# Optimization experiments

Measured on AMD Instinct MI355X. Metric: run time of the kernel, lower is better.

The kernel has to match this reference:

```python
import jax, jax.numpy as jnp
import numpy as np

NQ, NT, NA = 10000, 50000, 50000
E_GR, E_LT, E_SIM, E_COMP, E_GEN = 50000, 50000, 80000, 100000, 50000
HID, NH, HC, DOT, NL = 512, 4, 128, 256, 2
NEG_SLOPE = 0.2  # PyG GATv2Conv default negative_slope


def _gatv2(x_src, x_dst, src, dst, Wl, bl, Wr, br, att, bias, n_dst):
    # GATv2: x_j = lin_l(x_src), x_i = lin_r(x_dst); e = att . leaky_relu(x_i + x_j)
    xl = (x_src @ Wl + bl).reshape(-1, NH, HC)   # [Ns,H,C]
    xr = (x_dst @ Wr + br).reshape(-1, NH, HC)   # [Nd,H,C]
    m = jax.nn.leaky_relu(xl[src] + xr[dst], NEG_SLOPE)      # [E,H,C]
    logits = jnp.einsum('ehc,hc->eh', m, att)                # [E,H]
    lmax = jax.lax.stop_gradient(jax.ops.segment_max(logits, dst, num_segments=n_dst))
    lmax = jnp.where(jnp.isfinite(lmax), lmax, 0.0)
    ex = jnp.exp(logits - lmax[dst])
    denom = jax.ops.segment_sum(ex, dst, num_segments=n_dst)
    alpha = ex / (denom[dst] + 1e-16)                        # softmax over incoming edges
    out = jax.ops.segment_sum(xl[src] * alpha[:, :, None], dst, num_segments=n_dst)
    return out.reshape(n_dst, NH * HC) + bias


def _layernorm(x, g, b):
    mu = x.mean(-1, keepdims=True)
    var = ((x - mu) ** 2).mean(-1, keepdims=True)
    return (x - mu) / jnp.sqrt(var + 1e-5) * g + b


def _forward(xq, xt, xa, answer_features,
             qp_W, qp_b, tp_W, tp_b, ap_W, ap_b,
             afp_W1, afp_b1, afp_W2, afp_b2,
             conv_Wl, conv_bl, conv_Wr, conv_br, conv_att, conv_bias,
             qh_W, qh_b, qh_g, qh_beta, rh_W, rh_b, rh_g, rh_beta, score_bias,
             ei_gr, ei_lt, ei_sim, ei_comp, ei_gen):
    hq = xq @ qp_W + qp_b
    ht = xt @ tp_W + tp_b
    ha = xa @ ap_W + ap_b
    # add_self_loops=True only for ('query','similar_to','query')
    loops = jnp.arange(NQ, dtype=ei_sim.dtype)
    sim_src = jnp.concatenate([ei_sim[0], loops])
    sim_dst = jnp.concatenate([ei_sim[1], loops])
    for l in range(NL):
        P = lambda r: (conv_Wl[l, r], conv_bl[l, r], conv_Wr[l, r], conv_br[l, r], conv_att[l, r], conv_bias[l, r])
        o_gr = _gatv2(hq, ht, ei_gr[0], ei_gr[1], *P(0), NT)          # query -> think
        o_rgr = _gatv2(ht, hq, ei_gr[1], ei_gr[0], *P(1), NQ)         # think -> query (rev)
        o_lt = _gatv2(ht, ha, ei_lt[0], ei_lt[1], *P(2), NA)          # think -> answer
        o_rlt = _gatv2(ha, ht, ei_lt[1], ei_lt[0], *P(3), NT)         # answer -> think (rev)
        o_sim = _gatv2(hq, hq, sim_src, sim_dst, *P(4), NQ)           # query -> query
        o_cmp = _gatv2(ht, ht, ei_comp[0], ei_comp[1], *P(5), NT)     # think -> think
        # HeteroConv aggr='mean' across relations per destination type, then relu
        hq = jax.nn.relu((o_rgr + o_sim) / 2.0)
        ht = jax.nn.relu((o_gr + o_rlt + o_cmp) / 3.0)
        ha = jax.nn.relu(o_lt)
    q_emb = hq[ei_gen[0]]
    a_emb = ha[ei_gen[1]]
    t_emb = ht[ei_gen[1]]  # faithful to source: think indexed with answer-side index
    af_emb = jax.nn.relu(answer_features @ afp_W1 + afp_b1) @ afp_W2 + afp_b2
    q = _layernorm(q_emb @ qh_W + qh_b, qh_g, qh_beta)
    r = _layernorm(jnp.concatenate([t_emb, a_emb, af_emb], -1) @ rh_W + rh_b, rh_g, rh_beta)
    return (q * r).sum(-1) / jnp.sqrt(jnp.float32(DOT)) + score_bias


def setup_inputs() -> dict:
    ks = jax.random.split(jax.random.key(0), 40)
    n = lambda j, shape, s=0.05: jax.random.normal(ks[j], shape, jnp.float32) * s
    ri = lambda j, shape, hi: jax.random.randint(ks[j], shape, 0, hi, jnp.int32)
    return dict(
        xq=n(0, (NQ, 384), 1.0), xt=n(1, (NT, 384), 1.0), xa=n(2, (NA, 384), 1.0),
        answer_features=n(3, (E_GEN, 6), 1.0),
        qp_W=n(4, (384, HID)), qp_b=n(5, (HID,)),
        tp_W=n(6, (384, HID)), tp_b=n(7, (HID,)),
        ap_W=n(8, (384, HID)), ap_b=n(9, (HID,)),
        afp_W1=n(10, (6, 64)), afp_b1=n(11, (64,)),
        afp_W2=n(12, (64, HID)), afp_b2=n(13, (HID,)),
        conv_Wl=n(14, (NL, 6, HID, HID)), conv_bl=n(15, (NL, 6, HID)),
        conv_Wr=n(16, (NL, 6, HID, HID)), conv_br=n(17, (NL, 6, HID)),
        conv_att=n(18, (NL, 6, NH, HC)), conv_bias=n(19, (NL, 6, HID)),
        qh_W=n(20, (HID, DOT)), qh_b=n(21, (DOT,)),
        qh_g=jnp.ones((DOT,), jnp.float32), qh_beta=jnp.zeros((DOT,), jnp.float32),
        rh_W=n(22, (HID * 3, DOT)), rh_b=n(23, (DOT,)),
        rh_g=jnp.ones((DOT,), jnp.float32), rh_beta=jnp.zeros((DOT,), jnp.float32),
        score_bias=jnp.zeros((1,), jnp.float32),
        ei_gr=jnp.stack([ri(24, (E_GR,), NQ), ri(25, (E_GR,), NT)]),
        ei_lt=jnp.stack([ri(26, (E_LT,), NT), ri(27, (E_LT,), NA)]),
        ei_sim=ri(28, (2, E_SIM), NQ),
        ei_comp=ri(29, (2, E_COMP), NT),
        ei_gen=jnp.stack([ri(30, (E_GEN,), NQ), ri(31, (E_GEN,), NA)]),
    )


def reference(xq, xt, xa, answer_features,
              qp_W, qp_b, tp_W, tp_b, ap_W, ap_b,
              afp_W1, afp_b1, afp_W2, afp_b2,
              conv_Wl, conv_bl, conv_Wr, conv_br, conv_att, conv_bias,
              qh_W, qh_b, qh_g, qh_beta, rh_W, rh_b, rh_g, rh_beta, score_bias,
              ei_gr, ei_lt, ei_sim, ei_comp, ei_gen):
    return _forward(xq, xt, xa, answer_features,
                    qp_W, qp_b, tp_W, tp_b, ap_W, ap_b,
                    afp_W1, afp_b1, afp_W2, afp_b2,
                    conv_Wl, conv_bl, conv_Wr, conv_br, conv_att, conv_bias,
                    qh_W, qh_b, qh_g, qh_beta, rh_W, rh_b, rh_g, rh_beta, score_bias,
                    ei_gr, ei_lt, ei_sim, ei_comp, ei_gen)
```

## Files before the change

kernel.cpp:

```cpp
#include <hip/hip_runtime.h>
#include <cstdio>
#include <type_traits>

#define NQ 10000
#define NT 50000
#define NA 50000
#define E_GR 50000
#define E_LT 50000
#define E_SIM 80000
#define E_COMP 100000
#define E_GEN 50000
#define NEG_SLOPE 0.2f

#define NDTOT 220000
#define NSTOT 220000
#define ETOT  390000
__device__ __constant__ const int c_degOff[7]  = {0, 50000, 60000, 110000, 120000, 170000, 220000};
__device__ __constant__ const int c_sOff[7]    = {0, 10000, 60000, 110000, 120000, 170000, 220000};
__device__ __constant__ const int c_eOff[7]    = {0, 50000, 100000, 150000, 240000, 340000, 390000};
__device__ __constant__ const int c_nb[6]      = {49, 10, 49, 10, 49, 49};
__device__ __constant__ const int c_nbOff[7]   = {0, 49, 59, 108, 118, 167, 216};
__device__ __constant__ const int c_snb[6]     = {10, 49, 49, 10, 49, 49};
__device__ __constant__ const int c_snbOff[7]  = {0, 10, 59, 108, 118, 167, 216};

typedef unsigned short bf16_t;
typedef unsigned int u32;
typedef __attribute__((ext_vector_type(8))) short short8v;
typedef __attribute__((ext_vector_type(4))) float f32x4;

__device__ __forceinline__ float bf2f(u32 bits) { return __uint_as_float(bits << 16); }
__device__ __forceinline__ u32 f2bf(float f) {
  u32 u = __float_as_uint(f);
  return (u + 0x7FFFu + ((u >> 16) & 1u)) >> 16;
}
__device__ __forceinline__ u32 pack2(float a, float b) { return f2bf(a) | (f2bf(b) << 16); }
__device__ __forceinline__ void unpack8(uint4 u, float* f) {
  f[0] = bf2f(u.x & 0xffffu); f[1] = bf2f(u.x >> 16);
  f[2] = bf2f(u.y & 0xffffu); f[3] = bf2f(u.y >> 16);
  f[4] = bf2f(u.z & 0xffffu); f[5] = bf2f(u.z >> 16);
  f[6] = bf2f(u.w & 0xffffu); f[7] = bf2f(u.w >> 16);
}

__device__ __forceinline__ void gload16(const void* g, void* l) {
  __builtin_amdgcn_global_load_lds(
      (const __attribute__((address_space(1))) void*)g,
      (__attribute__((address_space(3))) void*)l, 16, 0, 0);
}

struct GemmDesc {
  const bf16_t* A; const bf16_t* Bt; const float* bias; void* C;
  const int* ridx; int N; const int* Nc; int K;
};

template <typename CT>
__global__ __launch_bounds__(512, 4) void bgemm(
    GemmDesc d0, GemmDesc d1, GemmDesc d2, int M, int accumulate)
{
  __shared__ short lds[3][12288];
  const int z = blockIdx.z;
  GemmDesc d = (z == 2) ? d2 : (z == 1) ? d1 : d0;
  int N = d.Nc ? *d.Nc : d.N;
  const int K = d.K;

  const int tid = threadIdx.x;
  const int ncol = gridDim.x;
  const int nband = (N + 127) >> 7;
  int lin = blockIdx.y * ncol + blockIdx.x;
  if (lin >= ncol * nband) return;

  int band, col;
  const int full = (nband >> 3) * 8 * ncol;
  if (lin < full) {
    int g = lin >> 3, x = lin & 7;
    band = x + 8 * (g / ncol);
    col  = g % ncol;
  } else {
    int r = lin - full;
    band = (nband & ~7) + r / ncol;
    col  = r % ncol;
  }
  const int bm = band * 128, bn = col * 256;

  const int lane = tid & 63;
  const int w = tid >> 6;
  const int wr = w >> 2, wc = w & 3;
  const int fr = lane & 15, fg = lane >> 4;

  const int kg = (((tid & 3) ^ ((tid >> 3) & 3)) << 3);
  const int rr = tid >> 2;
  int ra = min(bm + rr, N - 1);
  const bf16_t* gA0 = d.A + (size_t)(d.ridx ? d.ridx[ra] : ra) * K + kg;
  const bf16_t* gB0 = d.Bt + (size_t)(bn + rr) * K + kg;
  const bf16_t* gB1 = d.Bt + (size_t)(bn + 128 + rr) * K + kg;
  const int wb = w << 9;

  f32x4 acc[4][4];
#pragma unroll
  for (int i = 0; i < 4; ++i)
#pragma unroll
    for (int j = 0; j < 4; ++j) acc[i][j] = (f32x4){0.f, 0.f, 0.f, 0.f};

  auto stage = [&](int buf, int k0) {
    short* base = &lds[buf][0];
    gload16(gA0 + k0, base + wb);
    gload16(gB0 + k0, base + 4096 + wb);
    gload16(gB1 + k0, base + 8192 + wb);
  };

  const int nsteps = K >> 5;
  stage(0, 0);
  const int co = (fg ^ ((fr >> 1) & 3)) << 3;
  for (int s = 0; s < nsteps; ++s) {
    const int cur = s % 3;
    if (s + 1 < nsteps) {
      stage((s + 1) % 3, (s + 1) << 5);
      asm volatile("s_waitcnt vmcnt(3)" ::: "memory");
    } else {
      asm volatile("s_waitcnt vmcnt(0)" ::: "memory");
    }
    __builtin_amdgcn_s_barrier();
    asm volatile("" ::: "memory");
    const short* LA = &lds[cur][0];
    const short* LB = &lds[cur][4096];
    short8v b[4];
#pragma unroll
    for (int j = 0; j < 4; ++j) {
      int R = wc * 64 + j * 16 + fr;
      b[j] = *(const short8v*)&LB[R * 32 + co];
    }
#pragma unroll
    for (int i = 0; i < 4; ++i) {
      int R = wr * 64 + i * 16 + fr;
      short8v a = *(const short8v*)&LA[R * 32 + co];
#pragma unroll
      for (int j = 0; j < 4; ++j)
        acc[i][j] = __builtin_amdgcn_mfma_f32_16x16x32_bf16(b[j], a,
                                                            acc[i][j], 0, 0, 0);
    }
    asm volatile("" ::: "memory");
  }

  CT* C = (CT*)d.C;
  float4 bv[4];
#pragma unroll
  for (int j = 0; j < 4; ++j) {
    bv[j] = make_float4(0.f, 0.f, 0.f, 0.f);
    if (!accumulate && d.bias)
      bv[j] = *(const float4*)(d.bias + bn + wc * 64 + j * 16 + fg * 4);
  }
#pragma unroll
  for (int i = 0; i < 4; ++i) {
    const int n = bm + wr * 64 + i * 16 + fr;
    if (n >= N) continue;
#pragma unroll
    for (int j = 0; j < 4; ++j) {
      const int m0 = bn + wc * 64 + j * 16 + fg * 4;
      f32x4 v = acc[i][j];
      if constexpr (std::is_same<CT, float>::value) {
        float* p = C + (size_t)n * M + m0;
        if (accumulate) {
          float4 o = *(float4*)p;
          o.x += v[0]; o.y += v[1]; o.z += v[2]; o.w += v[3];
          *(float4*)p = o;
        } else {
          *(float4*)p = make_float4(v[0] + bv[j].x, v[1] + bv[j].y,
                                    v[2] + bv[j].z, v[3] + bv[j].w);
        }
      } else {
        uint2 o;
        o.x = pack2(v[0] + bv[j].x, v[1] + bv[j].y);
        o.y = pack2(v[2] + bv[j].z, v[3] + bv[j].w);
        *(uint2*)(C + (size_t)n * M + m0) = o;
      }
    }
  }
}

__device__ __forceinline__ void wT_tile(
    const float* __restrict__ W, bf16_t* __restrict__ Wt, int K, int M)
{
  __shared__ float sm[32][33];
  int mb = blockIdx.x * 32, kb = blockIdx.y * 32;
  int tx = threadIdx.x & 31, ty = threadIdx.x >> 5;
#pragma unroll
  for (int i = 0; i < 4; ++i)
    sm[ty + i * 8][tx] = W[(size_t)(kb + ty + i * 8) * M + mb + tx];
  __syncthreads();
#pragma unroll
  for (int i = 0; i < 4; ++i)
    Wt[(size_t)(mb + ty + i * 8) * K + kb + tx] = (bf16_t)f2bf(sm[tx][ty + i * 8]);
}

__global__ __launch_bounds__(256) void convert_wT(
    const float* __restrict__ W, bf16_t* __restrict__ Wt, int K, int M)
{
  wT_tile(W + (size_t)blockIdx.z * K * M, Wt + (size_t)blockIdx.z * K * M, K, M);
}
__global__ __launch_bounds__(256) void convert_wT24(
    const float* __restrict__ Wl, bf16_t* __restrict__ wl,
    const float* __restrict__ Wr, bf16_t* __restrict__ wr)
{
  int z = blockIdx.z;
  size_t o = (size_t)(z < 12 ? z : z - 12) * 512 * 512;
  if (z < 12) wT_tile(Wl + o, wl + o, 512, 512);
  else        wT_tile(Wr + o, wr + o, 512, 512);
}
__global__ __launch_bounds__(256) void convert_wT3(
    const float* __restrict__ W0, const float* __restrict__ W1,
    const float* __restrict__ W2, bf16_t* __restrict__ T0,
    bf16_t* __restrict__ T1, bf16_t* __restrict__ T2)
{
  int z = blockIdx.z;
  const float* W = z == 0 ? W0 : z == 1 ? W1 : W2;
  bf16_t* T = z == 0 ? T0 : z == 1 ? T1 : T2;
  wT_tile(W, T, 384, 512);
}
__global__ __launch_bounds__(256) void convert_wT4h(
    const float* __restrict__ qh, const float* __restrict__ rh,
    bf16_t* __restrict__ wqh, bf16_t* __restrict__ wrh)
{
  int z = blockIdx.z;
  if (z == 0) wT_tile(qh, wqh, 512, 256);
  else        wT_tile(rh + (size_t)(z - 1) * 512 * 256,
                      wrh + (size_t)(z - 1) * 256 * 512, 512, 256);
}

__global__ __launch_bounds__(256) void cast_flat(
    const float* __restrict__ in, bf16_t* __restrict__ out, int n4)
{
  int t = blockIdx.x * 256 + threadIdx.x;
  if (t >= n4) return;
  float4 v = ((const float4*)in)[t];
  uint2 o;
  o.x = pack2(v.x, v.y);
  o.y = pack2(v.z, v.w);
  ((uint2*)out)[t] = o;
}

__global__ __launch_bounds__(256) void fold_cvec(
    const float* __restrict__ b2, const float* __restrict__ rh2,
    float* __restrict__ cvec)
{
  int m = threadIdx.x;
  float s = 0.f;
  for (int k = 0; k < 512; ++k) s = fmaf(b2[k], rh2[(size_t)k * 256 + m], s);
  cvec[m] = s;
}

#define N4_XQ (NQ * 96)
#define N4_XT (NT * 96)
#define N4_XA (NA * 96)
__global__ __launch_bounds__(256) void cast3(
    const float* __restrict__ xq, const float* __restrict__ xt,
    const float* __restrict__ xa, bf16_t* __restrict__ xqb,
    bf16_t* __restrict__ xtb, bf16_t* __restrict__ xab)
{
  long g = (long)blockIdx.x * 256 + threadIdx.x;
  const float* in; bf16_t* out; long idx;
  if (g < N4_XQ)                { in = xq; out = xqb; idx = g; }
  else if (g < N4_XQ + N4_XT)   { in = xt; out = xtb; idx = g - N4_XQ; }
  else if (g < N4_XQ + N4_XT + N4_XA) { in = xa; out = xab; idx = g - N4_XQ - N4_XT; }
  else return;
  float4 v = ((const float4*)in)[idx];
  uint2 o;
  o.x = pack2(v.x, v.y);
  o.y = pack2(v.z, v.w);
  ((uint2*)out)[idx] = o;
}

__global__ __launch_bounds__(256) void combine_bias6(
    const float* __restrict__ cb, float* __restrict__ bcAll)
{
  int g = blockIdx.x * 256 + threadIdx.x;
  if (g >= 6 * 512) return;
  int row = g >> 9, j = g & 511;
  int l = row / 3, kind = row % 3;
  const float* b = cb + (size_t)l * 6 * 512;
  float v;
  if (kind == 0)      v = (b[0 * 512 + j] + b[3 * 512 + j] + b[5 * 512 + j]) / 3.f;
  else if (kind == 1) v = (b[1 * 512 + j] + b[4 * 512 + j]) * 0.5f;
  else                v = b[2 * 512 + j];
  bcAll[(size_t)row * 512 + j] = v;
}

__device__ __forceinline__ int find_rel6(int g, const int* off) {
  int r = 0;
#pragma unroll
  for (int k = 1; k < 6; ++k) r += (g >= off[k]);
  return r;
}

__global__ __launch_bounds__(256) void hist6(
    const int* __restrict__ d0, const int* __restrict__ d1,
    const int* __restrict__ d2, const int* __restrict__ d3,
    const int* __restrict__ d4, const int* __restrict__ d5,
    const int* __restrict__ s0p, const int* __restrict__ s1p,
    const int* __restrict__ s2p, const int* __restrict__ s3p,
    const int* __restrict__ s4p, const int* __restrict__ s5p,
    int* __restrict__ degAll, int* __restrict__ sdegAll, int* __restrict__ pos)
{
  int g = blockIdx.x * 256 + threadIdx.x;
  if (g >= ETOT) return;
  int r = find_rel6(g, c_eOff);
  int le = g - c_eOff[r];
  const int* dp = r == 0 ? d0 : r == 1 ? d1 : r == 2 ? d2 : r == 3 ? d3
                : r == 4 ? d4 : d5;
  const int* sp = r == 0 ? s0p : r == 1 ? s1p : r == 2 ? s2p : r == 3 ? s3p
                : r == 4 ? s4p : s5p;
  pos[g] = atomicAdd(&degAll[c_degOff[r] + dp[le]], 1);
  atomicAdd(&sdegAll[c_sOff[r] + sp[le]], 1);
}

__global__ __launch_bounds__(256) void scan1All(
    const int* __restrict__ degAll, const int* __restrict__ sdegAll,
    int* __restrict__ startAll, int* __restrict__ cposAll,
    int* __restrict__ sposAll, int* __restrict__ bsumAll)
{
  __shared__ int sm[256];
  int j = blockIdx.x / 216, bb = blockIdx.x % 216;
  const int* nbOff = (j == 2) ? c_snbOff : c_nbOff;
  const int* dOff  = (j == 2) ? c_sOff : c_degOff;
  const int* in    = (j == 2) ? sdegAll : degAll;
  int* out = j == 0 ? startAll : j == 1 ? cposAll : sposAll;
  int r = 0;
#pragma unroll
  for (int k = 1; k < 6; ++k) r += (bb >= nbOff[k]);
  int lb = bb - nbOff[r];
  int base0 = dOff[r], n = dOff[r + 1] - base0;
  int t = threadIdx.x;
  int base = lb * 1024 + t * 4;
  int v[4], sum = 0;
#pragma unroll
  for (int k = 0; k < 4; ++k) {
    int raw = (base + k < n) ? in[base0 + base + k] : 0;
    v[k] = j == 0 ? raw : j == 1 ? (raw >= 2 ? 1 : 0) : (raw >= 1 ? 1 : 0);
    sum += v[k];
  }
  sm[t] = sum;
  __syncthreads();
  for (int off = 1; off < 256; off <<= 1) {
    int x = (t >= off) ? sm[t - off] : 0;
    __syncthreads();
    sm[t] += x;
    __syncthreads();
  }
  int run = (t > 0) ? sm[t - 1] : 0;
  if (t == 255) bsumAll[j * 384 + r * 64 + lb] = sm[255];
#pragma unroll
  for (int k = 0; k < 4; ++k) {
    if (base + k < n) out[base0 + base + k] = run;
    run += v[k];
  }
}

__global__ __launch_bounds__(64) void scan2All(
    int* __restrict__ bsumAll, int* __restrict__ ccount, int* __restrict__ scount)
{
  __shared__ int sm[64];
  int j = blockIdx.x / 6, r = blockIdx.x % 6;
  int nb = (j == 2) ? c_snb[r] : c_nb[r];
  int t = threadIdx.x;
  int v = (t < nb) ? bsumAll[j * 384 + r * 64 + t] : 0;
  sm[t] = v;
  __syncthreads();
  for (int off = 1; off < 64; off <<= 1) {
    int x = (t >= off) ? sm[t - off] : 0;
    __syncthreads();
    sm[t] += x;
    __syncthreads();
  }
  if (t < nb) bsumAll[j * 384 + r * 64 + t] = sm[t] - v;
  if (t == nb - 1) {
    if (j == 1) ccount[r] = sm[t];
    if (j == 2) scount[r] = sm[t];
  }
}

__global__ __launch_bounds__(256) void scan3All(
    int* __restrict__ startAll, int* __restrict__ cposAll,
    int* __restrict__ sposAll, const int* __restrict__ bsumAll)
{
  int g = blockIdx.x * 256 + threadIdx.x;
  if (g >= 3 * NDTOT) return;
  int j = g / NDTOT, ln0 = g % NDTOT;
  const int* dOff = (j == 2) ? c_sOff : c_degOff;
  int* out = j == 0 ? startAll : j == 1 ? cposAll : sposAll;
  int r = find_rel6(ln0, dOff);
  int ln = ln0 - dOff[r];
  out[ln0] += bsumAll[j * 384 + r * 64 + (ln >> 10)];
}

__global__ __launch_bounds__(256) void scatter6(
    const int* __restrict__ d0, const int* __restrict__ d1,
    const int* __restrict__ d2, const int* __restrict__ d3,
    const int* __restrict__ d4, const int* __restrict__ d5,
    const int* __restrict__ s0p, const int* __restrict__ s1p,
    const int* __restrict__ s2p, const int* __restrict__ s3p,
    const int* __restrict__ s4p, const int* __restrict__ s5p,
    const int* __restrict__ startAll, const int* __restrict__ pos,
    const int* __restrict__ sposAll,
    int* __restrict__ eidxAll, int* __restrict__ srcCAll)
{
  int g = blockIdx.x * 256 + threadIdx.x;
  if (g >= ETOT) return;
  int r = find_rel6(g, c_eOff);
  int le = g - c_eOff[r];
  const int* dp = r == 0 ? d0 : r == 1 ? d1 : r == 2 ? d2 : r == 3 ? d3
                : r == 4 ? d4 : d5;
  const int* sp = r == 0 ? s0p : r == 1 ? s1p : r == 2 ? s2p : r == 3 ? s3p
                : r == 4 ? s4p : s5p;
  eidxAll[c_eOff[r] + startAll[c_degOff[r] + dp[le]] + pos[g]] = le;
  srcCAll[g] = sposAll[c_sOff[r] + sp[le]];
}

__global__ __launch_bounds__(256) void compactBoth(
    const int* __restrict__ degAll, const int* __restrict__ cposAll,
    int* __restrict__ cidxAll,
    const int* __restrict__ sdegAll, const int* __restrict__ sposAll,
    int* __restrict__ sidxAll)
{
  int g = blockIdx.x * 256 + threadIdx.x;
  if (g < NDTOT) {
    if (degAll[g] >= 2) {
      int r = find_rel6(g, c_degOff);
      cidxAll[c_degOff[r] + cposAll[g]] = g - c_degOff[r];
    }
  } else if (g < NDTOT + NSTOT) {
    int h = g - NDTOT;
    if (sdegAll[h] >= 1) {
      int r = find_rel6(h, c_sOff);
      sidxAll[c_sOff[r] + sposAll[h]] = h - c_sOff[r];
    }
  }
}

__global__ __launch_bounds__(256) void gat_fused(
    const bf16_t* __restrict__ xl, const bf16_t* __restrict__ xr,
    const int* __restrict__ srcC, const int* __restrict__ start,
    const int* __restrict__ deg, const int* __restrict__ eidx,
    const int* __restrict__ cpos, const float* __restrict__ att,
    bf16_t* __restrict__ acc, int Nd, int accumulate,
    const float* __restrict__ bc, float inv_div)
{
  int d = blockIdx.x * 4 + (threadIdx.x >> 6);
  if (d >= Nd) return;
  int lane = threadIdx.x & 63;

  float acc8[8] = {0.f, 0.f, 0.f, 0.f, 0.f, 0.f, 0.f, 0.f};
  int n = deg[d], s0 = start[d];
  if (n == 1) {
    int s = srcC[eidx[s0]];
    unpack8(*(const uint4*)(xl + (size_t)s * 512 + lane * 8), acc8);
  } else if (n > 1) {
    float xrr[8];
    unpack8(*(const uint4*)(xr + (size_t)cpos[d] * 512 + lane * 8), xrr);
    float at[8];
    *(float4*)(at)     = *(const float4*)(att + lane * 8);
    *(float4*)(at + 4) = *(const float4*)(att + lane * 8 + 4);
    float den = 0.f;
    int sN = srcC[eidx[s0]];
    for (int i = 0; i < n; ++i) {
      int s = sN;
      if (i + 1 < n) sN = srcC[eidx[s0 + i + 1]];
      float f[8];
      unpack8(*(const uint4*)(xl + (size_t)s * 512 + lane * 8), f);
      float p = 0.f;
#pragma unroll
      for (int k = 0; k < 8; ++k) {
        float x = f[k] + xrr[k];
        p = fmaf(at[k], x >= 0.f ? x : NEG_SLOPE * x, p);
      }
#pragma unroll
      for (int m = 8; m >= 1; m >>= 1) p += __shfl_xor(p, m);
      float ex = __expf(p);
      den += ex;
#pragma unroll
      for (int k = 0; k < 8; ++k) acc8[k] = fmaf(ex, f[k], acc8[k]);
    }
    float inv = 1.f / (den + 1e-16f);
#pragma unroll
    for (int k = 0; k < 8; ++k) acc8[k] *= inv;
  }

  bf16_t* out = acc + (size_t)d * 512 + lane * 8;
  if (accumulate) {
    float old[8];
    unpack8(*(const uint4*)out, old);
#pragma unroll
    for (int k = 0; k < 8; ++k) acc8[k] += old[k];
  }
  if (bc) {
    float bcv[8];
    *(float4*)(bcv)     = *(const float4*)(bc + lane * 8);
    *(float4*)(bcv + 4) = *(const float4*)(bc + lane * 8 + 4);
#pragma unroll
    for (int k = 0; k < 8; ++k)
      acc8[k] = fmaxf(fmaf(acc8[k], inv_div, bcv[k]), 0.f);
  }
  uint4 s;
  s.x = pack2(acc8[0], acc8[1]); s.y = pack2(acc8[2], acc8[3]);
  s.z = pack2(acc8[4], acc8[5]); s.w = pack2(acc8[6], acc8[7]);
  *(uint4*)out = s;
}

__global__ __launch_bounds__(256) void af_hidden(
    const float* __restrict__ af, const float* __restrict__ W1,
    const float* __restrict__ b1, bf16_t* __restrict__ out, int n)
{
  int t = blockIdx.x * blockDim.x + threadIdx.x;
  if (t >= n * 64) return;
  int i = t >> 6, j = t & 63;
  const float* a = af + (size_t)i * 6;
  float s = b1[j];
#pragma unroll
  for (int k = 0; k < 6; ++k) s = fmaf(a[k], W1[k * 64 + j], s);
  out[t] = (bf16_t)f2bf(fmaxf(s, 0.f));
}

__global__ __launch_bounds__(256) void build_sim(
    const int* __restrict__ ei, int* __restrict__ ss, int* __restrict__ sd)
{
  int t = blockIdx.x * blockDim.x + threadIdx.x;
  if (t >= E_SIM + NQ) return;
  if (t < E_SIM) { ss[t] = ei[t]; sd[t] = ei[E_SIM + t]; }
  else           { ss[t] = t - E_SIM; sd[t] = t - E_SIM; }
}

__global__ __launch_bounds__(256) void head_final(
    const float* __restrict__ qn, const float* __restrict__ rn,
    const float* __restrict__ afr, const float* __restrict__ cvec,
    const int* __restrict__ gsrc, const int* __restrict__ gdst,
    const float* __restrict__ qg, const float* __restrict__ qb,
    const float* __restrict__ rg, const float* __restrict__ rb,
    const float* __restrict__ score_bias, float* __restrict__ out, int E)
{
  int e = blockIdx.x * 4 + (threadIdx.x >> 6);
  if (e >= E) return;
  int lane = threadIdx.x & 63;

  float4 q = *(const float4*)(qn + (size_t)gsrc[e] * 256 + lane * 4);
  float s = q.x + q.y + q.z + q.w;
#pragma unroll
  for (int m = 32; m >= 1; m >>= 1) s += __shfl_xor(s, m);
  float mu = s * (1.f / 256.f);
  float dq0 = q.x - mu, dq1 = q.y - mu, dq2 = q.z - mu, dq3 = q.w - mu;
  float v = dq0 * dq0 + dq1 * dq1 + dq2 * dq2 + dq3 * dq3;
#pragma unroll
  for (int m = 32; m >= 1; m >>= 1) v += __shfl_xor(v, m);
  float rstd = rsqrtf(v * (1.f / 256.f) + 1e-5f);
  float4 g4 = *(const float4*)(qg + lane * 4);
  float4 b4 = *(const float4*)(qb + lane * 4);
  float qn0 = dq0 * rstd * g4.x + b4.x, qn1 = dq1 * rstd * g4.y + b4.y;
  float qn2 = dq2 * rstd * g4.z + b4.z, qn3 = dq3 * rstd * g4.w + b4.w;

  float4 r0 = *(const float4*)(rn + (size_t)gdst[e] * 256 + lane * 4);
  float4 r1 = *(const float4*)(afr + (size_t)e * 256 + lane * 4);
  float4 cv = *(const float4*)(cvec + lane * 4);
  float4 r;
  r.x = r0.x + r1.x + cv.x;
  r.y = r0.y + r1.y + cv.y;
  r.z = r0.z + r1.z + cv.z;
  r.w = r0.w + r1.w + cv.w;
  s = r.x + r.y + r.z + r.w;
#pragma unroll
  for (int m = 32; m >= 1; m >>= 1) s += __shfl_xor(s, m);
  mu = s * (1.f / 256.f);
  float dr0 = r.x - mu, dr1 = r.y - mu, dr2 = r.z - mu, dr3 = r.w - mu;
  v = dr0 * dr0 + dr1 * dr1 + dr2 * dr2 + dr3 * dr3;
#pragma unroll
  for (int m = 32; m >= 1; m >>= 1) v += __shfl_xor(v, m);
  rstd = rsqrtf(v * (1.f / 256.f) + 1e-5f);
  g4 = *(const float4*)(rg + lane * 4);
  b4 = *(const float4*)(rb + lane * 4);
  float rn0 = dr0 * rstd * g4.x + b4.x, rn1 = dr1 * rstd * g4.y + b4.y;
  float rn2 = dr2 * rstd * g4.z + b4.z, rn3 = dr3 * rstd * g4.w + b4.w;

  float d = qn0 * rn0 + qn1 * rn1 + qn2 * rn2 + qn3 * rn3;
#pragma unroll
  for (int m = 32; m >= 1; m >>= 1) d += __shfl_xor(d, m);
  if (lane == 0) out[e] = d * 0.0625f + score_bias[0];
}

extern "C" void kernel_launch(void* const* d_in, const int* in_sizes, int n_in,
                              void* d_out, int out_size, void* d_ws, size_t ws_size,
                              hipStream_t stream) {
  (void)in_sizes; (void)n_in; (void)out_size;
  const float* xq      = (const float*)d_in[0];
  const float* xt      = (const float*)d_in[1];
  const float* xa      = (const float*)d_in[2];
  const float* af      = (const float*)d_in[3];
  const float* qp_W    = (const float*)d_in[4];
  const float* qp_b    = (const float*)d_in[5];
  const float* tp_W    = (const float*)d_in[6];
  const float* tp_b    = (const float*)d_in[7];
  const float* ap_W    = (const float*)d_in[8];
  const float* ap_b    = (const float*)d_in[9];
  const float* afp_W1  = (const float*)d_in[10];
  const float* afp_b1  = (const float*)d_in[11];
  const float* afp_W2  = (const float*)d_in[12];
  const float* afp_b2  = (const float*)d_in[13];
  const float* conv_Wl = (const float*)d_in[14];
  const float* conv_bl = (const float*)d_in[15];
  const float* conv_Wr = (const float*)d_in[16];
  const float* conv_br = (const float*)d_in[17];
  const float* conv_att  = (const float*)d_in[18];
  const float* conv_bias = (const float*)d_in[19];
  const float* qh_W    = (const float*)d_in[20];
  const float* qh_b    = (const float*)d_in[21];
  const float* qh_g    = (const float*)d_in[22];
  const float* qh_beta = (const float*)d_in[23];
  const float* rh_W    = (const float*)d_in[24];
  const float* rh_b    = (const float*)d_in[25];
  const float* rh_g    = (const float*)d_in[26];
  const float* rh_beta = (const float*)d_in[27];
  const float* score_b = (const float*)d_in[28];
  const int* ei_gr   = (const int*)d_in[29];
  const int* ei_lt   = (const int*)d_in[30];
  const int* ei_sim  = (const int*)d_in[31];
  const int* ei_comp = (const int*)d_in[32];
  const int* ei_gen  = (const int*)d_in[33];

  char* base = (char*)d_ws;
  size_t off = 0;
  auto alloc = [&](size_t bytes) {
    void* p = base + off;
    off = (off + bytes + 255) & ~(size_t)255;
    return p;
  };
  bf16_t* hq   = (bf16_t*)alloc((size_t)NQ * 512 * 2);
  bf16_t* ht   = (bf16_t*)alloc((size_t)NT * 512 * 2);
  bf16_t* ha   = (bf16_t*)alloc((size_t)NA * 512 * 2);
  bf16_t* acct = (bf16_t*)alloc((size_t)NT * 512 * 2);
  bf16_t* accq = (bf16_t*)alloc((size_t)NQ * 512 * 2);
  bf16_t* xlb  = (bf16_t*)alloc((size_t)50000 * 512 * 2);
  bf16_t* xrb  = (bf16_t*)alloc((size_t)50000 * 512 * 2);
  int* simsrc  = (int*)alloc((size_t)(E_SIM + NQ) * 4);
  int* simdst  = (int*)alloc((size_t)(E_SIM + NQ) * 4);

  bf16_t* wqp  = (bf16_t*)alloc((size_t)512 * 384 * 2);
  bf16_t* wtp  = (bf16_t*)alloc((size_t)512 * 384 * 2);
  bf16_t* wap  = (bf16_t*)alloc((size_t)512 * 384 * 2);
  bf16_t* wl   = (bf16_t*)alloc((size_t)12 * 512 * 512 * 2);
  bf16_t* wr   = (bf16_t*)alloc((size_t)12 * 512 * 512 * 2);
  bf16_t* wqh  = (bf16_t*)alloc((size_t)256 * 512 * 2);
  bf16_t* wrh0 = (bf16_t*)alloc((size_t)256 * 512 * 2);
  bf16_t* wrh1 = (bf16_t*)alloc((size_t)256 * 512 * 2);
  bf16_t* wrh2 = (bf16_t*)alloc((size_t)256 * 512 * 2);
  float* bcAll = (float*)alloc(6 * 512 * 4);
  bf16_t* a2b    = (bf16_t*)alloc((size_t)64 * 512 * 2);
  float*  wfoldF = (float*)alloc((size_t)64 * 256 * 4);
  bf16_t* wfoldT = (bf16_t*)alloc((size_t)256 * 64 * 2);
  float*  cvec   = (float*)alloc(256 * 4);

  int* degAll   = (int*)alloc((size_t)NDTOT * 4);
  int* sdegAll  = (int*)alloc((size_t)NSTOT * 4);
  int* startAll = (int*)alloc((size_t)NDTOT * 4);
  int* cposAll  = (int*)alloc((size_t)NDTOT * 4);
  int* cidxAll  = (int*)alloc((size_t)NDTOT * 4);
  int* sposAll  = (int*)alloc((size_t)NSTOT * 4);
  int* sidxAll  = (int*)alloc((size_t)NSTOT * 4);
  int* eidxAll  = (int*)alloc((size_t)ETOT * 4);
  int* srcCAll  = (int*)alloc((size_t)ETOT * 4);
  int* posb     = (int*)alloc((size_t)ETOT * 4);
  int* bsumAll  = (int*)alloc(3 * 6 * 64 * 4);
  int* ccount   = (int*)alloc(6 * 4);
  int* scount   = (int*)alloc(6 * 4);
  if (off > ws_size) {
    fprintf(stderr, "kernel_launch: ws too small, need %zu have %zu\n", off, ws_size);
    return;
  }

  const int degOff[6] = {0, 50000, 60000, 110000, 120000, 170000};
  const int sOff[6]   = {0, 10000, 60000, 110000, 120000, 170000};
  const int eOff[6]   = {0, 50000, 100000, 150000, 240000, 340000};

  auto mkDesc = [](const bf16_t* A, const bf16_t* Bt, const float* bias, void* C,
                   const int* ridx, int N, const int* Nc, int K) {
    GemmDesc d; d.A = A; d.Bt = Bt; d.bias = bias; d.C = C;
    d.ridx = ridx; d.N = N; d.Nc = Nc; d.K = K; return d;
  };
  GemmDesc dz = mkDesc(nullptr, nullptr, nullptr, nullptr, nullptr, 0, nullptr, 32);

  auto launch_b = [&](GemmDesc a, GemmDesc b, GemmDesc c, int nz, int maxN,
                      int M, int acc_) {
    dim3 g(M / 256, (maxN + 127) / 128, nz);
    bgemm<bf16_t><<<g, 512, 0, stream>>>(a, b, c, M, acc_);
  };
  auto launch_f = [&](GemmDesc a, GemmDesc b, GemmDesc c, int nz, int maxN,
                      int M, int acc_) {
    dim3 g(M / 256, (maxN + 127) / 128, nz);
    bgemm<float><<<g, 512, 0, stream>>>(a, b, c, M, acc_);
  };

  convert_wT24<<<dim3(16, 16, 24), 256, 0, stream>>>(conv_Wl, wl, conv_Wr, wr);
  convert_wT3<<<dim3(16, 12, 3), 256, 0, stream>>>(qp_W, tp_W, ap_W, wqp, wtp, wap);
  convert_wT4h<<<dim3(8, 16, 4), 256, 0, stream>>>(qh_W, rh_W, wqh, wrh0);
  combine_bias6<<<(6 * 512 + 255) / 256, 256, 0, stream>>>(conv_bias, bcAll);
  cast_flat<<<(64 * 512 / 4 + 255) / 256, 256, 0, stream>>>(afp_W2, a2b, 64 * 512 / 4);
  launch_f(mkDesc(a2b, wrh2, nullptr, wfoldF, nullptr, 64, nullptr, 512),
           dz, dz, 1, 64, 256, 0);
  convert_wT<<<dim3(8, 2, 1), 256, 0, stream>>>(wfoldF, wfoldT, 64, 256);
  fold_cvec<<<1, 256, 0, stream>>>(afp_b2, rh_W + 1024 * 256, cvec);

  build_sim<<<(E_SIM + NQ + 255) / 256, 256, 0, stream>>>(ei_sim, simsrc, simdst);
  const int* dsts[6]  = {ei_gr + E_GR, ei_gr, ei_lt, simdst,
                         ei_comp + E_COMP, ei_lt + E_LT};
  const int* srcsA[6] = {ei_gr, ei_gr + E_GR, ei_lt + E_LT, simsrc,
                         ei_comp, ei_lt};
  hipMemsetAsync(degAll, 0, (size_t)(sdegAll + NSTOT) - (size_t)degAll, stream);
  hist6<<<(ETOT + 255) / 256, 256, 0, stream>>>(
      dsts[0], dsts[1], dsts[2], dsts[3], dsts[4], dsts[5],
      srcsA[0], srcsA[1], srcsA[2], srcsA[3], srcsA[4], srcsA[5],
      degAll, sdegAll, posb);
  scan1All<<<648, 256, 0, stream>>>(degAll, sdegAll, startAll, cposAll,
                                    sposAll, bsumAll);
  scan2All<<<18, 64, 0, stream>>>(bsumAll, ccount, scount);
  scan3All<<<(3 * NDTOT + 255) / 256, 256, 0, stream>>>(startAll, cposAll,
                                                        sposAll, bsumAll);
  scatter6<<<(ETOT + 255) / 256, 256, 0, stream>>>(
      dsts[0], dsts[1], dsts[2], dsts[3], dsts[4], dsts[5],
      srcsA[0], srcsA[1], srcsA[2], srcsA[3], srcsA[4], srcsA[5],
      startAll, posb, sposAll, eidxAll, srcCAll);
  compactBoth<<<(NDTOT + NSTOT + 255) / 256, 256, 0, stream>>>(
      degAll, cposAll, cidxAll, sdegAll, sposAll, sidxAll);

  cast3<<<((long)(N4_XQ + N4_XT + N4_XA) + 255) / 256, 256, 0, stream>>>(
      xq, xt, xa, accq, xlb, xrb);
  launch_b(mkDesc(accq, wqp, qp_b, hq, nullptr, NQ, nullptr, 384),
           mkDesc(xlb, wtp, tp_b, ht, nullptr, NT, nullptr, 384),
           mkDesc(xrb, wap, ap_b, ha, nullptr, NA, nullptr, 384),
           3, NT, 512, 0);

  const int NdArr[6] = {NT, NQ, NT, NQ, NT, NA};
  const int NsArr[6] = {NQ, NT, NA, NQ, NT, NT};
  bf16_t *hq_i = hq, *ht_i = ht, *hq_o = accq, *ht_o = acct;
  for (int l = 0; l < 2; ++l) {
    const float* bc_t = bcAll + (size_t)(l * 3 + 0) * 512;
    const float* bc_q = bcAll + (size_t)(l * 3 + 1) * 512;
    const float* bc_a = bcAll + (size_t)(l * 3 + 2) * 512;

    struct Rel { const bf16_t* xs; const bf16_t* xd; int po; bf16_t* acc;
                 int accum; const float* bc; float inv; };
    Rel rels[6] = {
      {hq_i, ht_i, 0, ht_o, 0, nullptr, 0.f},
      {ht_i, hq_i, 1, hq_o, 0, nullptr, 0.f},
      {ha,   ht_i, 3, ht_o, 1, nullptr, 0.f},
      {hq_i, hq_i, 4, hq_o, 1, bc_q, 0.5f},
      {ht_i, ht_i, 5, ht_o, 1, bc_t, 1.f / 3.f},
      {ht_i, ha,   2, ha,   0, bc_a, 1.f},
    };
    for (int r = 0; r < 6; ++r) {
      const Rel& R = rels[r];
      int Nd_ = NdArr[r];
      size_t po = (size_t)l * 6 + R.po;
      int maxN = NsArr[r] > Nd_ ? NsArr[r] : Nd_;
      launch_b(mkDesc(R.xs, wl + po * 512 * 512, conv_bl + po * 512, xlb,
                      sidxAll + sOff[r], NsArr[r], scount + r, 512),
               mkDesc(R.xd, wr + po * 512 * 512, conv_br + po * 512, xrb,
                      cidxAll + degOff[r], Nd_, ccount + r, 512),
               dz, 2, maxN, 512, 0);
      int gb = (Nd_ + 3) / 4;
      gat_fused<<<gb, 256, 0, stream>>>(xlb, xrb, srcCAll + eOff[r],
                                        startAll + degOff[r], degAll + degOff[r],
                                        eidxAll + eOff[r], cposAll + degOff[r],
                                        conv_att + po * 512,
                                        R.acc, Nd_, R.accum, R.bc, R.inv);
    }
    bf16_t* t;
    t = hq_i; hq_i = hq_o; hq_o = t;
    t = ht_i; ht_i = ht_o; ht_o = t;
  }

  float* qn  = (float*)accq;
  float* rn  = (float*)acct;
  float* afr = (float*)xrb;
  bf16_t* afh = xlb;
  const int* gsrc = ei_gen;
  const int* gdst = ei_gen + E_GEN;

  af_hidden<<<(E_GEN * 64 + 255) / 256, 256, 0, stream>>>(af, afp_W1, afp_b1,
                                                          afh, E_GEN);
  launch_f(mkDesc(hq_i, wqh, qh_b, qn, nullptr, NQ, nullptr, 512),
           mkDesc(ht_i, wrh0, rh_b, rn, nullptr, NT, nullptr, 512),
           mkDesc(afh, wfoldT, nullptr, afr, nullptr, E_GEN, nullptr, 64),
           3, NT, 256, 0);
  launch_f(mkDesc(ha, wrh1, nullptr, rn, nullptr, NA, nullptr, 512),
           dz, dz, 1, NA, 256, 1);
  head_final<<<(E_GEN + 3) / 4, 256, 0, stream>>>(
      qn, rn, afr, cvec, gsrc, gdst,
      qh_g, qh_beta, rh_g, rh_beta, score_b, (float*)d_out, E_GEN);
}
```

Before: 1.192 ms.

## Batch projection GEMMs of paired relations into four-way grouped launches

Extends the grouped GEMM kernel to four descriptors and carves the two projection buffers into one arena with per-relation row offsets. Projections for relations 0 and 1, and for 2 and 3, now run in a single launch each, so six GEMM launches per layer become four. The goal is better GPU fill for the small query-side GEMMs and less launch and tail overhead. It depends on the compacted row counts fitting the hardcoded region sizes (for example 25000 rows for some destination sets), which would break if more distinct nodes appear.

```diff
diff --git a/kernel.cpp b/kernel.cpp
--- a/kernel.cpp
+++ b/kernel.cpp
@@ -54,11 +54,11 @@
 
 template <typename CT>
 __global__ __launch_bounds__(512, 4) void bgemm(
-    GemmDesc d0, GemmDesc d1, GemmDesc d2, int M, int accumulate)
+    GemmDesc d0, GemmDesc d1, GemmDesc d2, GemmDesc d3, int M, int accumulate)
 {
   __shared__ short lds[3][12288];
   const int z = blockIdx.z;
-  GemmDesc d = (z == 2) ? d2 : (z == 1) ? d1 : d0;
+  GemmDesc d = (z == 3) ? d3 : (z == 2) ? d2 : (z == 1) ? d1 : d0;
   int N = d.Nc ? *d.Nc : d.N;
   const int K = d.K;
 
@@ -632,8 +632,9 @@
   bf16_t* ha   = (bf16_t*)alloc((size_t)NA * 512 * 2);
   bf16_t* acct = (bf16_t*)alloc((size_t)NT * 512 * 2);
   bf16_t* accq = (bf16_t*)alloc((size_t)NQ * 512 * 2);
-  bf16_t* xlb  = (bf16_t*)alloc((size_t)50000 * 512 * 2);
-  bf16_t* xrb  = (bf16_t*)alloc((size_t)50000 * 512 * 2);
+  bf16_t* arena = (bf16_t*)alloc((size_t)100000 * 512 * 2);
+  bf16_t* xlb  = arena;
+  bf16_t* xrb  = arena + (size_t)50000 * 512;
   int* simsrc  = (int*)alloc((size_t)(E_SIM + NQ) * 4);
   int* simdst  = (int*)alloc((size_t)(E_SIM + NQ) * 4);
 
@@ -673,6 +674,7 @@
   const int degOff[6] = {0, 50000, 60000, 110000, 120000, 170000};
   const int sOff[6]   = {0, 10000, 60000, 110000, 120000, 170000};
   const int eOff[6]   = {0, 50000, 100000, 150000, 240000, 340000};
+  auto ROWS = [&](int r) { return arena + (size_t)r * 512; };
 
   auto mkDesc = [](const bf16_t* A, const bf16_t* Bt, const float* bias, void* C,
                    const int* ridx, int N, const int* Nc, int K) {
@@ -681,15 +683,15 @@
   };
   GemmDesc dz = mkDesc(nullptr, nullptr, nullptr, nullptr, nullptr, 0, nullptr, 32);
 
-  auto launch_b = [&](GemmDesc a, GemmDesc b, GemmDesc c, int nz, int maxN,
-                      int M, int acc_) {
+  auto launch_b = [&](GemmDesc a, GemmDesc b, GemmDesc c, GemmDesc d, int nz,
+                      int maxN, int M, int acc_) {
     dim3 g(M / 256, (maxN + 127) / 128, nz);
-    bgemm<bf16_t><<<g, 512, 0, stream>>>(a, b, c, M, acc_);
+    bgemm<bf16_t><<<g, 512, 0, stream>>>(a, b, c, d, M, acc_);
   };
-  auto launch_f = [&](GemmDesc a, GemmDesc b, GemmDesc c, int nz, int maxN,
-                      int M, int acc_) {
+  auto launch_f = [&](GemmDesc a, GemmDesc b, GemmDesc c, GemmDesc d, int nz,
+                      int maxN, int M, int acc_) {
     dim3 g(M / 256, (maxN + 127) / 128, nz);
-    bgemm<float><<<g, 512, 0, stream>>>(a, b, c, M, acc_);
+    bgemm<float><<<g, 512, 0, stream>>>(a, b, c, d, M, acc_);
   };
 
   convert_wT24<<<dim3(16, 16, 24), 256, 0, stream>>>(conv_Wl, wl, conv_Wr, wr);
@@ -698,7 +700,7 @@
   combine_bias6<<<(6 * 512 + 255) / 256, 256, 0, stream>>>(conv_bias, bcAll);
   cast_flat<<<(64 * 512 / 4 + 255) / 256, 256, 0, stream>>>(afp_W2, a2b, 64 * 512 / 4);
   launch_f(mkDesc(a2b, wrh2, nullptr, wfoldF, nullptr, 64, nullptr, 512),
-           dz, dz, 1, 64, 256, 0);
+           dz, dz, dz, 1, 64, 256, 0);
   convert_wT<<<dim3(8, 2, 1), 256, 0, stream>>>(wfoldF, wfoldT, 64, 256);
   fold_cvec<<<1, 256, 0, stream>>>(afp_b2, rh_W + 1024 * 256, cvec);
 
@@ -729,43 +731,66 @@
   launch_b(mkDesc(accq, wqp, qp_b, hq, nullptr, NQ, nullptr, 384),
            mkDesc(xlb, wtp, tp_b, ht, nullptr, NT, nullptr, 384),
            mkDesc(xrb, wap, ap_b, ha, nullptr, NA, nullptr, 384),
-           3, NT, 512, 0);
-
-  const int NdArr[6] = {NT, NQ, NT, NQ, NT, NA};
-  const int NsArr[6] = {NQ, NT, NA, NQ, NT, NT};
+           dz, 3, NT, 512, 0);
+
   bf16_t *hq_i = hq, *ht_i = ht, *hq_o = accq, *ht_o = acct;
   for (int l = 0; l < 2; ++l) {
     const float* bc_t = bcAll + (size_t)(l * 3 + 0) * 512;
     const float* bc_q = bcAll + (size_t)(l * 3 + 1) * 512;
     const float* bc_a = bcAll + (size_t)(l * 3 + 2) * 512;
-
-    struct Rel { const bf16_t* xs; const bf16_t* xd; int po; bf16_t* acc;
-                 int accum; const float* bc; float inv; };
-    Rel rels[6] = {
-      {hq_i, ht_i, 0, ht_o, 0, nullptr, 0.f},
-      {ht_i, hq_i, 1, hq_o, 0, nullptr, 0.f},
-      {ha,   ht_i, 3, ht_o, 1, nullptr, 0.f},
-      {hq_i, hq_i, 4, hq_o, 1, bc_q, 0.5f},
-      {ht_i, ht_i, 5, ht_o, 1, bc_t, 1.f / 3.f},
-      {ht_i, ha,   2, ha,   0, bc_a, 1.f},
+    size_t p0 = (size_t)l * 6 + 0;
+    size_t p1 = (size_t)l * 6 + 1;
+    size_t p3 = (size_t)l * 6 + 3;
+    size_t p4 = (size_t)l * 6 + 4;
+    size_t p5 = (size_t)l * 6 + 5;
+    size_t p2 = (size_t)l * 6 + 2;
+
+    auto gat = [&](int r, const bf16_t* xl_, const bf16_t* xr_, size_t po,
+                   bf16_t* acc_, int Nd_, int accum, const float* bc, float inv) {
+      gat_fused<<<(Nd_ + 3) / 4, 256, 0, stream>>>(
+          xl_, xr_, srcCAll + eOff[r], startAll + degOff[r], degAll + degOff[r],
+          eidxAll + eOff[r], cposAll + degOff[r], conv_att + po * 512,
+          acc_, Nd_, accum, bc, inv);
     };
-    for (int r = 0; r < 6; ++r) {
-      const Rel& R = rels[r];
-      int Nd_ = NdArr[r];
-      size_t po = (size_t)l * 6 + R.po;
-      int maxN = NsArr[r] > Nd_ ? NsArr[r] : Nd_;
-      launch_b(mkDesc(R.xs, wl + po * 512 * 512, conv_bl + po * 512, xlb,
-                      sidxAll + sOff[r], NsArr[r], scount + r, 512),
-               mkDesc(R.xd, wr + po * 512 * 512, conv_br + po * 512, xrb,
-                      cidxAll + degOff[r], Nd_, ccount + r, 512),
-               dz, 2, maxN, 512, 0);
-      int gb = (Nd_ + 3) / 4;
-      gat_fused<<<gb, 256, 0, stream>>>(xlb, xrb, srcCAll + eOff[r],
-                                        startAll + degOff[r], degAll + degOff[r],
-                                        eidxAll + eOff[r], cposAll + degOff[r],
-                                        conv_att + po * 512,
-                                        R.acc, Nd_, R.accum, R.bc, R.inv);
-    }
+
+    launch_b(mkDesc(hq_i, wl + p0 * 262144, conv_bl + p0 * 512, ROWS(0),
+                    sidxAll + sOff[0], 10000, scount + 0, 512),
+             mkDesc(ht_i, wr + p0 * 262144, conv_br + p0 * 512, ROWS(10000),
+                    cidxAll + degOff[0], 25000, ccount + 0, 512),
+             mkDesc(ht_i, wl + p1 * 262144, conv_bl + p1 * 512, ROWS(35000),
+                    sidxAll + sOff[1], 50000, scount + 1, 512),
+             mkDesc(hq_i, wr + p1 * 262144, conv_br + p1 * 512, ROWS(85000),
+                    cidxAll + degOff[1], 10000, ccount + 1, 512),
+             4, 50000, 512, 0);
+    gat(0, ROWS(0), ROWS(10000), p0, ht_o, NT, 0, nullptr, 0.f);
+    gat(1, ROWS(35000), ROWS(85000), p1, hq_o, NQ, 0, nullptr, 0.f);
+
+    launch_b(mkDesc(ha, wl + p3 * 262144, conv_bl + p3 * 512, ROWS(0),
+                    sidxAll + sOff[2], 50000, scount + 2, 512),
+             mkDesc(ht_i, wr + p3 * 262144, conv_br + p3 * 512, ROWS(50000),
+                    cidxAll + degOff[2], 25000, ccount + 2, 512),
+             mkDesc(hq_i, wl + p4 * 262144, conv_bl + p4 * 512, ROWS(75000),
+                    sidxAll + sOff[3], 10000, scount + 3, 512),
+             mkDesc(hq_i, wr + p4 * 262144, conv_br + p4 * 512, ROWS(85000),
+                    cidxAll + degOff[3], 10000, ccount + 3, 512),
+             4, 50000, 512, 0);
+    gat(2, ROWS(0), ROWS(50000), p3, ht_o, NT, 1, nullptr, 0.f);
+    gat(3, ROWS(75000), ROWS(85000), p4, hq_o, NQ, 1, bc_q, 0.5f);
+
+    launch_b(mkDesc(ht_i, wl + p5 * 262144, conv_bl + p5 * 512, ROWS(0),
+                    sidxAll + sOff[4], 50000, scount + 4, 512),
+             mkDesc(ht_i, wr + p5 * 262144, conv_br + p5 * 512, ROWS(50000),
+                    cidxAll + degOff[4], 50000, ccount + 4, 512),
+             dz, dz, 2, 50000, 512, 0);
+    gat(4, ROWS(0), ROWS(50000), p5, ht_o, NT, 1, bc_t, 1.f / 3.f);
+
+    launch_b(mkDesc(ht_i, wl + p2 * 262144, conv_bl + p2 * 512, ROWS(0),
+                    sidxAll + sOff[5], 50000, scount + 5, 512),
+             mkDesc(ha, wr + p2 * 262144, conv_br + p2 * 512, ROWS(50000),
+                    cidxAll + degOff[5], 25000, ccount + 5, 512),
+             dz, dz, 2, 50000, 512, 0);
+    gat(5, ROWS(0), ROWS(50000), p2, ha, NA, 0, bc_a, 1.f);
+
     bf16_t* t;
     t = hq_i; hq_i = hq_o; hq_o = t;
     t = ht_i; ht_i = ht_o; ht_o = t;
@@ -783,9 +808,9 @@
   launch_f(mkDesc(hq_i, wqh, qh_b, qn, nullptr, NQ, nullptr, 512),
            mkDesc(ht_i, wrh0, rh_b, rn, nullptr, NT, nullptr, 512),
            mkDesc(afh, wfoldT, nullptr, afr, nullptr, E_GEN, nullptr, 64),
-           3, NT, 256, 0);
+           dz, 3, NT, 256, 0);
   launch_f(mkDesc(ha, wrh1, nullptr, rn, nullptr, NA, nullptr, 512),
-           dz, dz, 1, NA, 256, 1);
+           dz, dz, dz, 1, NA, 256, 1);
   head_final<<<(E_GEN + 3) / 4, 256, 0, stream>>>(
       qn, rn, afr, cvec, gsrc, gdst,
       qh_g, qh_beta, rh_g, rh_beta, score_b, (float*)d_out, E_GEN);
```

Result: faster. 1.156 ms (-3.0%).
